# Kernel optimization log

Measured on AMD Instinct MI355X. Metric: run time of the kernel, lower is better.

## Reference

```python
import jax, jax.numpy as jnp
import numpy as np

N_NODES = 100000
N_EDGES = 1600000
N_ADJS = 2
N_LAYERS = 3
D_IN = 128
H = 128           # hidden dim; last conv out = 256 / num_adjs = 128
N_GRAPHS = 1024


def setup_inputs() -> dict:
    key = jax.random.key(0)
    ks = jax.random.split(key, 12)
    x = jax.random.normal(ks[0], (N_NODES, D_IN), dtype=jnp.float32)
    edge_index = jax.random.randint(ks[1], (N_ADJS, 2, N_EDGES), 0, N_NODES, dtype=jnp.int32)
    batch = jnp.sort(jax.random.randint(ks[2], (N_NODES,), 0, N_GRAPHS, dtype=jnp.int32))
    s = 0.05
    lin0_w = jax.random.normal(ks[3], (D_IN, H), dtype=jnp.float32) * s
    lin0_b = jnp.zeros((H,), dtype=jnp.float32)
    conv_w = jax.random.normal(ks[4], (N_ADJS, N_LAYERS, H, H), dtype=jnp.float32) * s
    lin1_w = jax.random.normal(ks[5], (2 * H, H), dtype=jnp.float32) * s
    lin1_b = jnp.zeros((H,), dtype=jnp.float32)
    lin2_w = jax.random.normal(ks[6], (H, 1), dtype=jnp.float32) * s
    lin2_b = jnp.zeros((1,), dtype=jnp.float32)
    return {"x": x, "edge_index": edge_index, "batch": batch,
            "lin0_w": lin0_w, "lin0_b": lin0_b, "conv_w": conv_w,
            "lin1_w": lin1_w, "lin1_b": lin1_b, "lin2_w": lin2_w, "lin2_b": lin2_b}


def _gcn_conv(h, W, row, col, norm, n_nodes):
    # GCNConv (bias=False): out[i] = sum_{j->i} norm_e * (h @ W)[j]
    m = h @ W                                  # [N, H] dense transform first (PyG order)
    msg = m[row] * norm[:, None]               # [E+N, H] gather + edge scaling
    return jax.ops.segment_sum(msg, col, num_segments=n_nodes)


def reference(x, edge_index, batch, lin0_w, lin0_b, conv_w, lin1_w, lin1_b, lin2_w, lin2_b):
    n = x.shape[0]
    loops = jnp.arange(n, dtype=edge_index.dtype)
    x0 = jax.nn.relu(x @ lin0_w + lin0_b)      # lin0 + relu
    pooled = []
    for a in range(N_ADJS):
        # gcn_norm with self loops: deg over targets, norm = d^-1/2[row] * d^-1/2[col]
        row = jnp.concatenate([edge_index[a, 0], loops])
        col = jnp.concatenate([edge_index[a, 1], loops])
        deg = jax.ops.segment_sum(jnp.ones_like(col, dtype=x.dtype), col, num_segments=n)
        dis = jnp.where(deg > 0, jax.lax.rsqrt(jnp.maximum(deg, 1e-12)), 0.0)
        norm = dis[row] * dis[col]
        h = x0
        for l in range(N_LAYERS):
            h = jax.nn.relu(_gcn_conv(h, conv_w[a, l], row, col, norm, n))
        # global_add_pool: segment sum over graph ids
        pooled.append(jax.ops.segment_sum(h, batch, num_segments=N_GRAPHS))
    g = jnp.concatenate(pooled, axis=1)        # [G, 256]
    g = jax.nn.relu(g @ lin1_w + lin1_b)
    # dropout(p=0.5) is identity in eval mode
    return g @ lin2_w + lin2_b                 # [G, 1]
```

## Files before the change

### kernel.cpp

```cpp
#include <hip/hip_runtime.h>

#define NN 100000
#define NE 1600000
#define NADJ 2
#define NLAY 3
#define HD 128
#define NG 1024

#define EB   1563
#define NBUK 391
#define BPAD 400

typedef unsigned int uint32;
typedef unsigned short u16;

typedef __attribute__((ext_vector_type(8))) short bfrag8;
typedef __attribute__((ext_vector_type(4))) float f32x4;
typedef __attribute__((ext_vector_type(2))) float f32x2;

__device__ __forceinline__ u16 f2bf(float f) {
    uint32 u = __float_as_uint(f);
    u += 0x7FFFu + ((u >> 16) & 1u);
    return (u16)(u >> 16);
}
__device__ __forceinline__ float bflo(uint32 u) { return __uint_as_float(u << 16); }
__device__ __forceinline__ float bfhi(uint32 u) { return __uint_as_float(u & 0xFFFF0000u); }

__global__ __launch_bounds__(256) void prep(
    const float* __restrict__ x, const float* __restrict__ conv_w,
    const float* __restrict__ lin0_w, u16* __restrict__ xbf,
    u16* __restrict__ wt) {
    if (blockIdx.x < 6250) {
        int i = blockIdx.x * 256 + threadIdx.x;
        float4 a = ((const float4*)x)[i * 2];
        float4 b = ((const float4*)x)[i * 2 + 1];
        uint4 v;
        v.x = (uint32)f2bf(a.x) | ((uint32)f2bf(a.y) << 16);
        v.y = (uint32)f2bf(a.z) | ((uint32)f2bf(a.w) << 16);
        v.z = (uint32)f2bf(b.x) | ((uint32)f2bf(b.y) << 16);
        v.w = (uint32)f2bf(b.z) | ((uint32)f2bf(b.w) << 16);
        ((uint4*)xbf)[i] = v;
    } else {
        int bid = blockIdx.x - 6250;
        const float* W = (bid < 6) ? conv_w + (size_t)bid * HD * HD : lin0_w;
        u16* o = wt + (size_t)bid * HD * HD;
        for (int i = 0; i < 64; ++i) {
            int idx = i * 256 + threadIdx.x;
            int n = idx >> 7, k = idx & 127;
            o[idx] = f2bf(W[k * 128 + n]);
        }
    }
}

__global__ __launch_bounds__(256) void gemm_mfma(
    const u16* __restrict__ Abf, const u16* __restrict__ Wt,
    u16* __restrict__ outbf, const float* __restrict__ dis,
    const float* __restrict__ bias, int relu)
{
    const int wid = blockIdx.x * 4 + (threadIdx.x >> 6);
    const int lane = threadIdx.x & 63;
    const int row0 = (wid >> 1) * 64;
    if (row0 >= NN) return;
    const int wc = (wid & 1) * 64;
    const int lr = lane & 15, kg = lane >> 4;

    bfrag8 a[4][4];
    #pragma unroll
    for (int ks = 0; ks < 4; ++ks)
        #pragma unroll
        for (int i = 0; i < 4; ++i)
            a[ks][i] = *(const bfrag8*)&Wt[(size_t)(wc + i * 16 + lr) * 128
                                           + (ks * 4 + kg) * 8];

    const f32x4 z = {0.f, 0.f, 0.f, 0.f};
    f32x4 acc[4][4];
    #pragma unroll
    for (int j = 0; j < 4; ++j)
        #pragma unroll
        for (int i = 0; i < 4; ++i) acc[j][i] = z;

    #pragma unroll
    for (int ks = 0; ks < 4; ++ks) {
        bfrag8 b[4];
        #pragma unroll
        for (int j = 0; j < 4; ++j) {
            int r = min(row0 + j * 16 + lr, NN - 1);
            b[j] = *(const bfrag8*)&Abf[(size_t)r * 128 + (ks * 4 + kg) * 8];
        }
        #pragma unroll
        for (int j = 0; j < 4; ++j)
            #pragma unroll
            for (int i = 0; i < 4; ++i)
                acc[j][i] = __builtin_amdgcn_mfma_f32_16x16x32_bf16(
                    a[ks][i], b[j], acc[j][i], 0, 0, 0);
    }

    #pragma unroll
    for (int j = 0; j < 4; ++j) {
        int m = row0 + j * 16 + lr;
        if (m < NN) {
            float ds = dis ? dis[m] : 1.f;
            #pragma unroll
            for (int i = 0; i < 4; ++i) {
                int colb = wc + i * 16 + kg * 4;
                float4 bb = make_float4(0.f, 0.f, 0.f, 0.f);
                if (bias) bb = *(const float4*)&bias[colb];
                float v0 = acc[j][i][0] * ds + bb.x;
                float v1 = acc[j][i][1] * ds + bb.y;
                float v2 = acc[j][i][2] * ds + bb.z;
                float v3 = acc[j][i][3] * ds + bb.w;
                if (relu) {
                    v0 = fmaxf(v0, 0.f); v1 = fmaxf(v1, 0.f);
                    v2 = fmaxf(v2, 0.f); v3 = fmaxf(v3, 0.f);
                }
                uint2 pk;
                pk.x = (uint32)f2bf(v0) | ((uint32)f2bf(v1) << 16);
                pk.y = (uint32)f2bf(v2) | ((uint32)f2bf(v3) << 16);
                *(uint2*)&outbf[(size_t)m * 128 + colb] = pk;
            }
        }
    }
}


__global__ __launch_bounds__(256) void p1_count(
    const int* __restrict__ ei, int* __restrict__ bcnt)
{
    __shared__ int h[NBUK];
    int aa = blockIdx.x >= EB ? 1 : 0;
    int blk = blockIdx.x - aa * EB;
    const int* col = ei + (size_t)aa * 2 * NE + NE;
    int* bc = bcnt + (size_t)aa * EB * BPAD;
    int t = threadIdx.x;
    for (int q = t; q < NBUK; q += 256) h[q] = 0;
    __syncthreads();
    int base = blk * 1024 + t;
    #pragma unroll
    for (int u = 0; u < 4; ++u) {
        int e = base + u * 256;
        if (e < NE) atomicAdd(&h[col[e] >> 8], 1);
    }
    __syncthreads();
    for (int q = t; q < NBUK; q += 256)
        bc[blk * BPAD + q] = h[q];
}

__global__ __launch_bounds__(256) void p2a_scanblocks(
    const int* __restrict__ bcnt, int* __restrict__ pscan,
    int* __restrict__ btot)
{
    __shared__ int s[256];
    int aa = blockIdx.x >= NBUK ? 1 : 0;
    int b = blockIdx.x - aa * NBUK;
    const int* bc = bcnt + (size_t)aa * EB * BPAD;
    int* ps = pscan + (size_t)aa * EB * BPAD;
    int* bt = btot + aa * BPAD;
    int t = threadIdx.x;
    int v[7];
    int loc = 0;
    #pragma unroll
    for (int j = 0; j < 7; ++j) {
        int idx = t * 7 + j;
        v[j] = (idx < EB) ? bc[idx * BPAD + b] : 0;
        loc += v[j];
    }
    s[t] = loc;
    __syncthreads();
    for (int off = 1; off < 256; off <<= 1) {
        int u = (t >= off) ? s[t - off] : 0;
        __syncthreads();
        s[t] += u;
        __syncthreads();
    }
    int pre = s[t] - loc;
    #pragma unroll
    for (int j = 0; j < 7; ++j) {
        int idx = t * 7 + j;
        if (idx < EB) ps[idx * BPAD + b] = pre;
        pre += v[j];
    }
    if (t == 255) bt[b] = s[255];
}

__global__ __launch_bounds__(512) void p2b_scanbuckets(
    const int* __restrict__ btot, int* __restrict__ bbase)
{
    __shared__ int s[512];
    int aa = blockIdx.x;
    const int* bt = btot + aa * BPAD;
    int* bb = bbase + aa * (NBUK + 1);
    int t = threadIdx.x;
    int v = (t < NBUK) ? bt[t] : 0;
    s[t] = v;
    __syncthreads();
    for (int off = 1; off < 512; off <<= 1) {
        int u = (t >= off) ? s[t - off] : 0;
        __syncthreads();
        s[t] += u;
        __syncthreads();
    }
    if (t < NBUK) bb[t] = s[t] - v;
    if (t == NBUK - 1) bb[NBUK] = s[t];
}

__global__ __launch_bounds__(256) void p3_partition(
    const int* __restrict__ ei, const int* __restrict__ pscan,
    const int* __restrict__ bbase, uint2* __restrict__ part)
{
    __shared__ int spre[NBUK];
    __shared__ int cur[NBUK];
    int aa = blockIdx.x >= EB ? 1 : 0;
    int blk = blockIdx.x - aa * EB;
    const int* row = ei + (size_t)aa * 2 * NE;
    const int* col = row + NE;
    const int* ps = pscan + (size_t)aa * EB * BPAD;
    const int* bb = bbase + aa * (NBUK + 1);
    uint2* pt = part + (size_t)aa * NE;
    int t = threadIdx.x;
    for (int q = t; q < NBUK; q += 256) {
        spre[q] = bb[q] + ps[blk * BPAD + q];
        cur[q] = 0;
    }
    __syncthreads();
    int base = blk * 1024 + t;
    #pragma unroll
    for (int u = 0; u < 4; ++u) {
        int e = base + u * 256;
        if (e < NE) {
            int c = col[e];
            int b = c >> 8;
            int rk = atomicAdd(&cur[b], 1);
            pt[spre[b] + rk] = make_uint2((uint32)row[e], (uint32)c);
        }
    }
}

__global__ __launch_bounds__(256) void p4_csr(
    const uint2* __restrict__ part, const int* __restrict__ bbase,
    int* __restrict__ row_ptr, float* __restrict__ dis,
    int* __restrict__ csr_src)
{
    __shared__ int cnt[256];
    __shared__ int s[256];
    __shared__ int sexcl[256];
    __shared__ int cur[256];
    int aa = blockIdx.x >= NBUK ? 1 : 0;
    int b = blockIdx.x - aa * NBUK;
    const uint2* pt = part + (size_t)aa * NE;
    const int* bb = bbase + aa * (NBUK + 1);
    int* rp = row_ptr + (size_t)aa * (NN + 1);
    float* ds = dis + (size_t)aa * NN;
    int* cs = csr_src + (size_t)aa * NE;
    int t = threadIdx.x;
    int base = bb[b];
    int ecnt = bb[b + 1] - base;
    int n0 = b << 8;
    cnt[t] = 0;
    cur[t] = 0;
    __syncthreads();
    for (int i = t; i < ecnt; i += 256)
        atomicAdd(&cnt[pt[base + i].y - n0], 1);
    __syncthreads();
    int v = cnt[t];
    s[t] = v;
    __syncthreads();
    for (int off = 1; off < 256; off <<= 1) {
        int u = (t >= off) ? s[t - off] : 0;
        __syncthreads();
        s[t] += u;
        __syncthreads();
    }
    sexcl[t] = s[t] - v;
    int node = n0 + t;
    if (node < NN) {
        rp[node] = base + s[t] - v;
        ds[node] = rsqrtf((float)(v + 1));
    }
    if (b == 0 && t == 0) rp[NN] = NE;
    __syncthreads();
    for (int i = t; i < ecnt; i += 256) {
        uint2 p = pt[base + i];
        int li = (int)p.y - n0;
        int rk = atomicAdd(&cur[li], 1);
        cs[base + sexcl[li] + rk] = (int)p.x;
    }
}

__global__ __launch_bounds__(256) void agg_relu(
    const u16* __restrict__ mm, const int* __restrict__ row_ptr,
    const int* __restrict__ csr_src,
    const float* __restrict__ dis, u16* __restrict__ out)
{
    int wid = blockIdx.x * 4 + (threadIdx.x >> 6);
    int nodeA = wid * 2;
    if (nodeA >= NN) return;
    int nodeB = nodeA + 1;
    uint32 lane = threadIdx.x & 63;
    const uint32* mv = (const uint32*)mm;
    int lan16 = (int)(lane & 15);

    uint32 selfA = mv[(uint32)nodeA * 64u + lane];
    uint32 selfB = mv[(uint32)nodeB * 64u + lane];
    f32x2 accA, accB;
    accA.x = bflo(selfA); accA.y = bfhi(selfA);
    accB.x = bflo(selfB); accB.y = bfhi(selfB);
    int eA = row_ptr[nodeA], e1A = row_ptr[nodeA + 1];
    int eB = e1A,            e1B = row_ptr[nodeB + 1];

    while (eA + 16 <= e1A && eB + 16 <= e1B) {
        uint32 pA = (uint32)csr_src[eA + lan16];
        uint32 pB = (uint32)csr_src[eB + lan16];
        #pragma unroll
        for (int u = 0; u < 16; ++u) {
            uint32 sA = (uint32)__builtin_amdgcn_readlane((int)pA, u);
            uint32 sB = (uint32)__builtin_amdgcn_readlane((int)pB, u);
            uint32 vA = (mv + (size_t)sA * 64u)[lane];
            uint32 vB = (mv + (size_t)sB * 64u)[lane];
            f32x2 tA, tB;
            tA.x = bflo(vA); tA.y = bfhi(vA);
            tB.x = bflo(vB); tB.y = bfhi(vB);
            asm("v_pk_add_f32 %0, %0, %1" : "+v"(accA) : "v"(tA));
            asm("v_pk_add_f32 %0, %0, %1" : "+v"(accB) : "v"(tB));
        }
        eA += 16; eB += 16;
    }
    for (; eA + 16 <= e1A; eA += 16) {
        uint32 pA = (uint32)csr_src[eA + lan16];
        #pragma unroll
        for (int u = 0; u < 16; ++u) {
            uint32 sA = (uint32)__builtin_amdgcn_readlane((int)pA, u);
            uint32 vA = (mv + (size_t)sA * 64u)[lane];
            f32x2 tA;
            tA.x = bflo(vA); tA.y = bfhi(vA);
            asm("v_pk_add_f32 %0, %0, %1" : "+v"(accA) : "v"(tA));
        }
    }
    for (; eB + 16 <= e1B; eB += 16) {
        uint32 pB = (uint32)csr_src[eB + lan16];
        #pragma unroll
        for (int u = 0; u < 16; ++u) {
            uint32 sB = (uint32)__builtin_amdgcn_readlane((int)pB, u);
            uint32 vB = (mv + (size_t)sB * 64u)[lane];
            f32x2 tB;
            tB.x = bflo(vB); tB.y = bfhi(vB);
            asm("v_pk_add_f32 %0, %0, %1" : "+v"(accB) : "v"(tB));
        }
    }
    int remA = e1A - eA, remB = e1B - eB;
    if ((remA | remB) != 0) {
        if (remA > 0 && remB > 0 && remA <= 8 && remB <= 8) {
            uint32 pA = (uint32)csr_src[min(eA + (int)(lane & 7), e1A - 1)];
            uint32 pB = (uint32)csr_src[min(eB + (int)(lane & 7), e1B - 1)];
            #pragma unroll
            for (int u = 0; u < 8; ++u) {
                uint32 sA = (uint32)__builtin_amdgcn_readlane((int)pA, u);
                uint32 sB = (uint32)__builtin_amdgcn_readlane((int)pB, u);
                uint32 vA = (mv + (size_t)sA * 64u)[lane];
                uint32 vB = (mv + (size_t)sB * 64u)[lane];
                float mA = (eA + u < e1A) ? 1.f : 0.f;
                float mB = (eB + u < e1B) ? 1.f : 0.f;
                f32x2 tA, tB, kA, kB;
                tA.x = bflo(vA); tA.y = bfhi(vA); kA.x = mA; kA.y = mA;
                tB.x = bflo(vB); tB.y = bfhi(vB); kB.x = mB; kB.y = mB;
                asm("v_pk_fma_f32 %0, %1, %2, %0" : "+v"(accA) : "v"(tA), "v"(kA));
                asm("v_pk_fma_f32 %0, %1, %2, %0" : "+v"(accB) : "v"(tB), "v"(kB));
            }
        } else {
            uint32 pA = 0, pB = 0;
            if (remA > 0) pA = (uint32)csr_src[min(eA + lan16, e1A - 1)];
            if (remB > 0) pB = (uint32)csr_src[min(eB + lan16, e1B - 1)];
            if (remA > 0 && remB > 0) {
                #pragma unroll
                for (int u = 0; u < 16; ++u) {
                    uint32 sA = (uint32)__builtin_amdgcn_readlane((int)pA, u);
                    uint32 sB = (uint32)__builtin_amdgcn_readlane((int)pB, u);
                    uint32 vA = (mv + (size_t)sA * 64u)[lane];
                    uint32 vB = (mv + (size_t)sB * 64u)[lane];
                    float mA = (eA + u < e1A) ? 1.f : 0.f;
                    float mB = (eB + u < e1B) ? 1.f : 0.f;
                    f32x2 tA, tB, kA, kB;
                    tA.x = bflo(vA); tA.y = bfhi(vA); kA.x = mA; kA.y = mA;
                    tB.x = bflo(vB); tB.y = bfhi(vB); kB.x = mB; kB.y = mB;
                    asm("v_pk_fma_f32 %0, %1, %2, %0" : "+v"(accA) : "v"(tA), "v"(kA));
                    asm("v_pk_fma_f32 %0, %1, %2, %0" : "+v"(accB) : "v"(tB), "v"(kB));
                }
            } else if (remA > 0) {
                #pragma unroll
                for (int u = 0; u < 16; ++u) {
                    uint32 sA = (uint32)__builtin_amdgcn_readlane((int)pA, u);
                    uint32 vA = (mv + (size_t)sA * 64u)[lane];
                    float mA = (eA + u < e1A) ? 1.f : 0.f;
                    f32x2 tA, kA;
                    tA.x = bflo(vA); tA.y = bfhi(vA); kA.x = mA; kA.y = mA;
                    asm("v_pk_fma_f32 %0, %1, %2, %0" : "+v"(accA) : "v"(tA), "v"(kA));
                }
            } else {
                #pragma unroll
                for (int u = 0; u < 16; ++u) {
                    uint32 sB = (uint32)__builtin_amdgcn_readlane((int)pB, u);
                    uint32 vB = (mv + (size_t)sB * 64u)[lane];
                    float mB = (eB + u < e1B) ? 1.f : 0.f;
                    f32x2 tB, kB;
                    tB.x = bflo(vB); tB.y = bfhi(vB); kB.x = mB; kB.y = mB;
                    asm("v_pk_fma_f32 %0, %1, %2, %0" : "+v"(accB) : "v"(tB), "v"(kB));
                }
            }
        }
    }

    float dA = dis[nodeA], dB = dis[nodeB];
    uint32 poA = (uint32)f2bf(fmaxf(dA * accA.x, 0.f))
               | ((uint32)f2bf(fmaxf(dA * accA.y, 0.f)) << 16);
    uint32 poB = (uint32)f2bf(fmaxf(dB * accB.x, 0.f))
               | ((uint32)f2bf(fmaxf(dB * accB.y, 0.f)) << 16);
    ((uint32*)out)[(uint32)nodeA * 64u + lane] = poA;
    ((uint32*)out)[(uint32)nodeB * 64u + lane] = poB;
}

__global__ __launch_bounds__(64) void pool_add(
    const u16* __restrict__ h, const int* __restrict__ batch,
    float* __restrict__ pooled, int aoff)
{
    int c2 = threadIdx.x;
    const uint32* hv = (const uint32*)h;
    int n0 = blockIdx.x * 64;
    int nend = min(n0 + 64, NN);
    int cur = batch[n0];
    float ax = 0.f, ay = 0.f;
    for (int n = n0; n < nend; ++n) {
        int g = batch[n];
        if (g != cur) {
            atomicAdd(&pooled[(size_t)cur * 256 + aoff + 2 * c2], ax);
            atomicAdd(&pooled[(size_t)cur * 256 + aoff + 2 * c2 + 1], ay);
            ax = 0.f; ay = 0.f;
            cur = g;
        }
        uint32 v = hv[(size_t)n * 64 + c2];
        ax += bflo(v);
        ay += bfhi(v);
    }
    atomicAdd(&pooled[(size_t)cur * 256 + aoff + 2 * c2], ax);
    atomicAdd(&pooled[(size_t)cur * 256 + aoff + 2 * c2 + 1], ay);
}

__global__ __launch_bounds__(128) void head(
    const float* __restrict__ pooled,
    const float* __restrict__ w1, const float* __restrict__ b1,
    const float* __restrict__ w2, const float* __restrict__ b2,
    float* __restrict__ out)
{
    __shared__ float sp[256];
    __shared__ float sg[128];
    int g = blockIdx.x, t = threadIdx.x;
    sp[t] = pooled[(size_t)g * 256 + t];
    sp[t + 128] = pooled[(size_t)g * 256 + 128 + t];
    __syncthreads();
    float acc = b1[t];
    #pragma unroll 8
    for (int k = 0; k < 256; ++k) acc = fmaf(sp[k], w1[k * 128 + t], acc);
    sg[t] = fmaxf(acc, 0.f) * w2[t];
    __syncthreads();
    for (int s2 = 64; s2 > 0; s2 >>= 1) {
        if (t < s2) sg[t] += sg[t + s2];
        __syncthreads();
    }
    if (t == 0) out[g] = sg[0] + b2[0];
}

extern "C" void kernel_launch(void* const* d_in, const int* in_sizes, int n_in,
                              void* d_out, int out_size, void* d_ws, size_t ws_size,
                              hipStream_t stream) {
    const float* x      = (const float*)d_in[0];
    const int*   ei     = (const int*)d_in[1];
    const int*   batch  = (const int*)d_in[2];
    const float* lin0_w = (const float*)d_in[3];
    const float* lin0_b = (const float*)d_in[4];
    const float* conv_w = (const float*)d_in[5];
    const float* lin1_w = (const float*)d_in[6];
    const float* lin1_b = (const float*)d_in[7];
    const float* lin2_w = (const float*)d_in[8];
    const float* lin2_b = (const float*)d_in[9];
    float* out = (float*)d_out;

    const size_t NB = (size_t)NN * HD;
    float* x0f    = (float*)d_ws;
    float* bufA   = x0f + NB;
    float* bufB   = bufA + NB;
    float* pooled = bufB + NB;
    int*   row_ptr2 = (int*)(pooled + (size_t)NG * 256);
    float* dis2     = (float*)(row_ptr2 + 2 * (NN + 1));
    int*   csr2     = (int*)(dis2 + 2 * NN);
    u16*   wt       = (u16*)(csr2 + 2 * NE);
    int*   bcnt2    = (int*)(wt + 7 * HD * HD);
    int*   pscan2   = bcnt2 + 2 * EB * BPAD;
    int*   btot2    = pscan2 + 2 * EB * BPAD;
    int*   bbase2   = btot2 + 2 * BPAD;

    u16* x0bf    = (u16*)x0f;
    u16* xbf     = (u16*)(x0f + NB / 2);
    u16* mm      = (u16*)bufA;
    uint2* part2 = (uint2*)(bufA + NB / 2);
    u16* hbuf    = (u16*)bufB;

    const int GEMM_BLOCKS = (((NN + 63) / 64) * 2 + 3) / 4;

    hipMemsetAsync(pooled, 0, (size_t)NG * 256 * sizeof(float), stream);

    prep<<<6250 + 7, 256, 0, stream>>>(x, conv_w, lin0_w, xbf, wt);

    p1_count<<<2 * EB, 256, 0, stream>>>(ei, bcnt2);
    p2a_scanblocks<<<2 * NBUK, 256, 0, stream>>>(bcnt2, pscan2, btot2);
    p2b_scanbuckets<<<2, 512, 0, stream>>>(btot2, bbase2);
    p3_partition<<<2 * EB, 256, 0, stream>>>(ei, pscan2, bbase2, part2);
    p4_csr<<<2 * NBUK, 256, 0, stream>>>(part2, bbase2, row_ptr2, dis2, csr2);

    gemm_mfma<<<GEMM_BLOCKS, 256, 0, stream>>>(
        xbf, wt + 6 * HD * HD, x0bf, nullptr, lin0_b, 1);

    for (int a = 0; a < NADJ; ++a) {
        const int*   rp = row_ptr2 + (size_t)a * (NN + 1);
        const float* ds = dis2 + (size_t)a * NN;
        const int*   cs = csr2 + (size_t)a * NE;

        const u16* h = x0bf;
        for (int l = 0; l < NLAY; ++l) {
            const u16* Wt = wt + ((size_t)a * NLAY + l) * HD * HD;
            gemm_mfma<<<GEMM_BLOCKS, 256, 0, stream>>>(h, Wt, mm, ds,
                                                       nullptr, 0);
            agg_relu<<<NN / 8, 256, 0, stream>>>(mm, rp, cs, ds, hbuf);
            h = hbuf;
        }
        pool_add<<<(NN + 63) / 64, 64, 0, stream>>>(hbuf, batch, pooled, a * HD);
    }

    head<<<NG, 128, 0, stream>>>(pooled, lin1_w, lin1_b, lin2_w, lin2_b, out);
}
```

Baseline: 696.6 us.

## Batch both adjacencies into single launches and coarsen edge bucketing

Merges the per-adjacency GEMM, aggregation and pooling launches so that each kernel processes both adjacency branches in one grid. This halves the kernel launch count and gives each launch twice the parallelism. The CSR build also uses 4096-edge blocks and 512-node buckets, which cuts the number of blocks and the size of the partial-scan tables. The partition buffer now aliases the h buffer, and each branch needs its own mm and h buffers of N×128 bf16, so workspace layout must hold.

```diff
diff --git a/kernel.cpp b/kernel.cpp
--- a/kernel.cpp
+++ b/kernel.cpp
@@ -7,9 +7,13 @@
 #define HD 128
 #define NG 1024
 
-#define EB   1563
-#define NBUK 391
-#define BPAD 400
+#define EBLK 4096
+#define EB   391
+#define NBUK 196
+#define BPAD 200
+#define GB   782
+#define AB   12500
+#define PB   1563
 
 typedef unsigned int uint32;
 typedef unsigned short u16;
@@ -54,8 +58,7 @@
 
 __global__ __launch_bounds__(256) void gemm_mfma(
     const u16* __restrict__ Abf, const u16* __restrict__ Wt,
-    u16* __restrict__ outbf, const float* __restrict__ dis,
-    const float* __restrict__ bias, int relu)
+    u16* __restrict__ outbf, const float* __restrict__ bias)
 {
     const int wid = blockIdx.x * 4 + (threadIdx.x >> 6);
     const int lane = threadIdx.x & 63;
@@ -99,23 +102,85 @@
     for (int j = 0; j < 4; ++j) {
         int m = row0 + j * 16 + lr;
         if (m < NN) {
-            float ds = dis ? dis[m] : 1.f;
             #pragma unroll
             for (int i = 0; i < 4; ++i) {
                 int colb = wc + i * 16 + kg * 4;
-                float4 bb = make_float4(0.f, 0.f, 0.f, 0.f);
-                if (bias) bb = *(const float4*)&bias[colb];
-                float v0 = acc[j][i][0] * ds + bb.x;
-                float v1 = acc[j][i][1] * ds + bb.y;
-                float v2 = acc[j][i][2] * ds + bb.z;
-                float v3 = acc[j][i][3] * ds + bb.w;
-                if (relu) {
-                    v0 = fmaxf(v0, 0.f); v1 = fmaxf(v1, 0.f);
-                    v2 = fmaxf(v2, 0.f); v3 = fmaxf(v3, 0.f);
-                }
+                float4 bb = *(const float4*)&bias[colb];
+                float v0 = fmaxf(acc[j][i][0] + bb.x, 0.f);
+                float v1 = fmaxf(acc[j][i][1] + bb.y, 0.f);
+                float v2 = fmaxf(acc[j][i][2] + bb.z, 0.f);
+                float v3 = fmaxf(acc[j][i][3] + bb.w, 0.f);
                 uint2 pk;
                 pk.x = (uint32)f2bf(v0) | ((uint32)f2bf(v1) << 16);
                 pk.y = (uint32)f2bf(v2) | ((uint32)f2bf(v3) << 16);
+                *(uint2*)&outbf[(size_t)m * 128 + colb] = pk;
+            }
+        }
+    }
+}
+
+__global__ __launch_bounds__(256) void gemm_mfma_b(
+    const u16* __restrict__ hbase, int shared, const u16* __restrict__ wt,
+    int l, u16* __restrict__ mm2, const float* __restrict__ dis2)
+{
+    int aa = blockIdx.x >= GB ? 1 : 0;
+    int bblk = blockIdx.x - aa * GB;
+    const u16* Abf = shared ? hbase : hbase + (size_t)aa * NN * HD;
+    const u16* Wt = wt + (size_t)(aa * NLAY + l) * HD * HD;
+    u16* outbf = mm2 + (size_t)aa * NN * HD;
+    const float* dis = dis2 + (size_t)aa * NN;
+
+    const int wid = bblk * 4 + (threadIdx.x >> 6);
+    const int lane = threadIdx.x & 63;
+    const int row0 = (wid >> 1) * 64;
+    if (row0 >= NN) return;
+    const int wc = (wid & 1) * 64;
+    const int lr = lane & 15, kg = lane >> 4;
+
+    bfrag8 a[4][4];
+    #pragma unroll
+    for (int ks = 0; ks < 4; ++ks)
+        #pragma unroll
+        for (int i = 0; i < 4; ++i)
+            a[ks][i] = *(const bfrag8*)&Wt[(size_t)(wc + i * 16 + lr) * 128
+                                           + (ks * 4 + kg) * 8];
+
+    const f32x4 z = {0.f, 0.f, 0.f, 0.f};
+    f32x4 acc[4][4];
+    #pragma unroll
+    for (int j = 0; j < 4; ++j)
+        #pragma unroll
+        for (int i = 0; i < 4; ++i) acc[j][i] = z;
+
+    #pragma unroll
+    for (int ks = 0; ks < 4; ++ks) {
+        bfrag8 b[4];
+        #pragma unroll
+        for (int j = 0; j < 4; ++j) {
+            int r = min(row0 + j * 16 + lr, NN - 1);
+            b[j] = *(const bfrag8*)&Abf[(size_t)r * 128 + (ks * 4 + kg) * 8];
+        }
+        #pragma unroll
+        for (int j = 0; j < 4; ++j)
+            #pragma unroll
+            for (int i = 0; i < 4; ++i)
+                acc[j][i] = __builtin_amdgcn_mfma_f32_16x16x32_bf16(
+                    a[ks][i], b[j], acc[j][i], 0, 0, 0);
+    }
+
+    #pragma unroll
+    for (int j = 0; j < 4; ++j) {
+        int m = row0 + j * 16 + lr;
+        if (m < NN) {
+            float ds = dis[m];
+            #pragma unroll
+            for (int i = 0; i < 4; ++i) {
+                int colb = wc + i * 16 + kg * 4;
+                uint2 pk;
+                pk.x = (uint32)f2bf(acc[j][i][0] * ds)
+                     | ((uint32)f2bf(acc[j][i][1] * ds) << 16);
+                pk.y = (uint32)f2bf(acc[j][i][2] * ds)
+                     | ((uint32)f2bf(acc[j][i][3] * ds) << 16);
                 *(uint2*)&outbf[(size_t)m * 128 + colb] = pk;
             }
         }
@@ -132,17 +197,16 @@
     const int* col = ei + (size_t)aa * 2 * NE + NE;
     int* bc = bcnt + (size_t)aa * EB * BPAD;
     int t = threadIdx.x;
-    for (int q = t; q < NBUK; q += 256) h[q] = 0;
-    __syncthreads();
-    int base = blk * 1024 + t;
-    #pragma unroll
-    for (int u = 0; u < 4; ++u) {
+    if (t < NBUK) h[t] = 0;
+    __syncthreads();
+    int base = blk * EBLK + t;
+    #pragma unroll
+    for (int u = 0; u < 16; ++u) {
         int e = base + u * 256;
-        if (e < NE) atomicAdd(&h[col[e] >> 8], 1);
-    }
-    __syncthreads();
-    for (int q = t; q < NBUK; q += 256)
-        bc[blk * BPAD + q] = h[q];
+        if (e < NE) atomicAdd(&h[col[e] >> 9], 1);
+    }
+    __syncthreads();
+    if (t < NBUK) bc[blk * BPAD + t] = h[t];
 }
 
 __global__ __launch_bounds__(256) void p2a_scanblocks(
@@ -156,11 +220,11 @@
     int* ps = pscan + (size_t)aa * EB * BPAD;
     int* bt = btot + aa * BPAD;
     int t = threadIdx.x;
-    int v[7];
+    int v[2];
     int loc = 0;
     #pragma unroll
-    for (int j = 0; j < 7; ++j) {
-        int idx = t * 7 + j;
+    for (int j = 0; j < 2; ++j) {
+        int idx = t * 2 + j;
         v[j] = (idx < EB) ? bc[idx * BPAD + b] : 0;
         loc += v[j];
     }
@@ -174,18 +238,18 @@
     }
     int pre = s[t] - loc;
     #pragma unroll
-    for (int j = 0; j < 7; ++j) {
-        int idx = t * 7 + j;
+    for (int j = 0; j < 2; ++j) {
+        int idx = t * 2 + j;
         if (idx < EB) ps[idx * BPAD + b] = pre;
         pre += v[j];
     }
     if (t == 255) bt[b] = s[255];
 }
 
-__global__ __launch_bounds__(512) void p2b_scanbuckets(
+__global__ __launch_bounds__(256) void p2b_scanbuckets(
     const int* __restrict__ btot, int* __restrict__ bbase)
 {
-    __shared__ int s[512];
+    __shared__ int s[256];
     int aa = blockIdx.x;
     const int* bt = btot + aa * BPAD;
     int* bb = bbase + aa * (NBUK + 1);
@@ -193,7 +257,7 @@
     int v = (t < NBUK) ? bt[t] : 0;
     s[t] = v;
     __syncthreads();
-    for (int off = 1; off < 512; off <<= 1) {
+    for (int off = 1; off < 256; off <<= 1) {
         int u = (t >= off) ? s[t - off] : 0;
         __syncthreads();
         s[t] += u;
@@ -217,18 +281,18 @@
     const int* bb = bbase + aa * (NBUK + 1);
     uint2* pt = part + (size_t)aa * NE;
     int t = threadIdx.x;
-    for (int q = t; q < NBUK; q += 256) {
-        spre[q] = bb[q] + ps[blk * BPAD + q];
-        cur[q] = 0;
-    }
-    __syncthreads();
-    int base = blk * 1024 + t;
-    #pragma unroll
-    for (int u = 0; u < 4; ++u) {
+    if (t < NBUK) {
+        spre[t] = bb[t] + ps[blk * BPAD + t];
+        cur[t] = 0;
+    }
+    __syncthreads();
+    int base = blk * EBLK + t;
+    #pragma unroll
+    for (int u = 0; u < 16; ++u) {
         int e = base + u * 256;
         if (e < NE) {
             int c = col[e];
-            int b = c >> 8;
+            int b = c >> 9;
             int rk = atomicAdd(&cur[b], 1);
             pt[spre[b] + rk] = make_uint2((uint32)row[e], (uint32)c);
         }
@@ -237,32 +301,33 @@
 
 __global__ __launch_bounds__(256) void p4_csr(
     const uint2* __restrict__ part, const int* __restrict__ bbase,
-    int* __restrict__ row_ptr, float* __restrict__ dis,
-    int* __restrict__ csr_src)
-{
-    __shared__ int cnt[256];
+    int* __restrict__ row_ptr2, float* __restrict__ dis2,
+    int* __restrict__ csr2)
+{
+    __shared__ int cnt[512];
+    __shared__ int sexcl[512];
+    __shared__ int cur[512];
     __shared__ int s[256];
-    __shared__ int sexcl[256];
-    __shared__ int cur[256];
     int aa = blockIdx.x >= NBUK ? 1 : 0;
     int b = blockIdx.x - aa * NBUK;
     const uint2* pt = part + (size_t)aa * NE;
     const int* bb = bbase + aa * (NBUK + 1);
-    int* rp = row_ptr + (size_t)aa * (NN + 1);
-    float* ds = dis + (size_t)aa * NN;
-    int* cs = csr_src + (size_t)aa * NE;
+    int* rp = row_ptr2 + (size_t)aa * (NN + 1);
+    float* ds = dis2 + (size_t)aa * NN;
+    int* cs = csr2 + (size_t)aa * NE;
     int t = threadIdx.x;
     int base = bb[b];
     int ecnt = bb[b + 1] - base;
-    int n0 = b << 8;
-    cnt[t] = 0;
-    cur[t] = 0;
+    int n0 = b << 9;
+    cnt[t] = 0; cnt[t + 256] = 0;
+    cur[t] = 0; cur[t + 256] = 0;
     __syncthreads();
     for (int i = t; i < ecnt; i += 256)
         atomicAdd(&cnt[pt[base + i].y - n0], 1);
     __syncthreads();
-    int v = cnt[t];
-    s[t] = v;
+    int c0 = cnt[2 * t], c1 = cnt[2 * t + 1];
+    int loc = c0 + c1;
+    s[t] = loc;
     __syncthreads();
     for (int off = 1; off < 256; off <<= 1) {
         int u = (t >= off) ? s[t - off] : 0;
@@ -270,11 +335,17 @@
         s[t] += u;
         __syncthreads();
     }
-    sexcl[t] = s[t] - v;
-    int node = n0 + t;
+    int pre = s[t] - loc;
+    sexcl[2 * t] = pre;
+    sexcl[2 * t + 1] = pre + c0;
+    int node = n0 + 2 * t;
     if (node < NN) {
-        rp[node] = base + s[t] - v;
-        ds[node] = rsqrtf((float)(v + 1));
+        rp[node] = base + pre;
+        ds[node] = rsqrtf((float)(c0 + 1));
+    }
+    if (node + 1 < NN) {
+        rp[node + 1] = base + pre + c0;
+        ds[node + 1] = rsqrtf((float)(c1 + 1));
     }
     if (b == 0 && t == 0) rp[NN] = NE;
     __syncthreads();
@@ -286,12 +357,20 @@
     }
 }
 
-__global__ __launch_bounds__(256) void agg_relu(
-    const u16* __restrict__ mm, const int* __restrict__ row_ptr,
-    const int* __restrict__ csr_src,
-    const float* __restrict__ dis, u16* __restrict__ out)
-{
-    int wid = blockIdx.x * 4 + (threadIdx.x >> 6);
+__global__ __launch_bounds__(256) void agg_relu_b(
+    const u16* __restrict__ mm2, const int* __restrict__ row_ptr2,
+    const int* __restrict__ csr2, const float* __restrict__ dis2,
+    u16* __restrict__ h2)
+{
+    int aa = blockIdx.x >= AB ? 1 : 0;
+    int blk = blockIdx.x - aa * AB;
+    const u16* mm = mm2 + (size_t)aa * NN * HD;
+    const int* row_ptr = row_ptr2 + (size_t)aa * (NN + 1);
+    const int* csr_src = csr2 + (size_t)aa * NE;
+    const float* dis = dis2 + (size_t)aa * NN;
+    u16* out = h2 + (size_t)aa * NN * HD;
+
+    int wid = blk * 4 + (threadIdx.x >> 6);
     int nodeA = wid * 2;
     if (nodeA >= NN) return;
     int nodeB = nodeA + 1;
@@ -417,13 +496,16 @@
     ((uint32*)out)[(uint32)nodeB * 64u + lane] = poB;
 }
 
-__global__ __launch_bounds__(64) void pool_add(
-    const u16* __restrict__ h, const int* __restrict__ batch,
-    float* __restrict__ pooled, int aoff)
-{
+__global__ __launch_bounds__(64) void pool_add_b(
+    const u16* __restrict__ h2, const int* __restrict__ batch,
+    float* __restrict__ pooled)
+{
+    int aa = blockIdx.x >= PB ? 1 : 0;
+    int blk = blockIdx.x - aa * PB;
+    const uint32* hv = (const uint32*)(h2 + (size_t)aa * NN * HD);
+    int aoff = aa * HD;
     int c2 = threadIdx.x;
-    const uint32* hv = (const uint32*)h;
-    int n0 = blockIdx.x * 64;
+    int n0 = blk * 64;
     int nend = min(n0 + 64, NN);
     int cur = batch[n0];
     float ax = 0.f, ay = 0.f;
@@ -498,11 +580,9 @@
 
     u16* x0bf    = (u16*)x0f;
     u16* xbf     = (u16*)(x0f + NB / 2);
-    u16* mm      = (u16*)bufA;
-    uint2* part2 = (uint2*)(bufA + NB / 2);
-    u16* hbuf    = (u16*)bufB;
-
-    const int GEMM_BLOCKS = (((NN + 63) / 64) * 2 + 3) / 4;
+    u16* mm2     = (u16*)bufA;
+    u16* h2      = (u16*)bufB;
+    uint2* part2 = (uint2*)bufB;
 
     hipMemsetAsync(pooled, 0, (size_t)NG * 256 * sizeof(float), stream);
 
@@ -510,28 +590,19 @@
 
     p1_count<<<2 * EB, 256, 0, stream>>>(ei, bcnt2);
     p2a_scanblocks<<<2 * NBUK, 256, 0, stream>>>(bcnt2, pscan2, btot2);
-    p2b_scanbuckets<<<2, 512, 0, stream>>>(btot2, bbase2);
+    p2b_scanbuckets<<<2, 256, 0, stream>>>(btot2, bbase2);
     p3_partition<<<2 * EB, 256, 0, stream>>>(ei, pscan2, bbase2, part2);
     p4_csr<<<2 * NBUK, 256, 0, stream>>>(part2, bbase2, row_ptr2, dis2, csr2);
 
-    gemm_mfma<<<GEMM_BLOCKS, 256, 0, stream>>>(
-        xbf, wt + 6 * HD * HD, x0bf, nullptr, lin0_b, 1);
-
-    for (int a = 0; a < NADJ; ++a) {
-        const int*   rp = row_ptr2 + (size_t)a * (NN + 1);
-        const float* ds = dis2 + (size_t)a * NN;
-        const int*   cs = csr2 + (size_t)a * NE;
-
-        const u16* h = x0bf;
-        for (int l = 0; l < NLAY; ++l) {
-            const u16* Wt = wt + ((size_t)a * NLAY + l) * HD * HD;
-            gemm_mfma<<<GEMM_BLOCKS, 256, 0, stream>>>(h, Wt, mm, ds,
-                                                       nullptr, 0);
-            agg_relu<<<NN / 8, 256, 0, stream>>>(mm, rp, cs, ds, hbuf);
-            h = hbuf;
-        }
-        pool_add<<<(NN + 63) / 64, 64, 0, stream>>>(hbuf, batch, pooled, a * HD);
-    }
+    gemm_mfma<<<GB, 256, 0, stream>>>(xbf, wt + 6 * HD * HD, x0bf, lin0_b);
+
+    for (int l = 0; l < NLAY; ++l) {
+        gemm_mfma_b<<<2 * GB, 256, 0, stream>>>(
+            l == 0 ? x0bf : h2, l == 0 ? 1 : 0, wt, l, mm2, dis2);
+        agg_relu_b<<<2 * AB, 256, 0, stream>>>(mm2, row_ptr2, csr2, dis2, h2);
+    }
+
+    pool_add_b<<<2 * PB, 64, 0, stream>>>(h2, batch, pooled);
 
     head<<<NG, 128, 0, stream>>>(pooled, lin1_w, lin1_b, lin2_w, lin2_b, out);
 }
```

New measurement: 620.0 us. 1.12x faster.
